# Kernel optimization log

Hardware: AMD Instinct MI355X
Metric: run time of the kernel (lower is better)

The kernel has to match this reference:

```python
import jax, jax.numpy as jnp
import numpy as np

N_NODES = 50000
N_EDGES = 800000
D_IN = 96
D_HID = 96


def _sage_conv(x, src, dst, Wl, b, Wr, n_nodes):
    # PyG SAGEConv (aggr='mean'): out = lin_l(mean_j x_j) + lin_r(x)
    msg = x[src]                                            # [E, d] gather
    agg = jax.ops.segment_sum(msg, dst, num_segments=n_nodes)
    cnt = jax.ops.segment_sum(jnp.ones((src.shape[0],), x.dtype), dst,
                              num_segments=n_nodes)
    agg = agg / jnp.maximum(cnt, 1.0)[:, None]              # mean (0 if no nbrs)
    return agg @ Wl.T + b + x @ Wr.T


def setup_inputs() -> dict:
    key = jax.random.key(0)
    ks = jax.random.split(key, 8)
    x = jax.random.normal(ks[0], (N_NODES, D_IN), dtype=jnp.float32)
    edge_index = jax.random.randint(ks[1], (2, N_EDGES), 0, N_NODES, dtype=jnp.int64)
    s1 = 1.0 / np.sqrt(D_IN)
    s2 = 1.0 / np.sqrt(D_HID)
    W1l = jax.random.uniform(ks[2], (D_HID, D_IN), jnp.float32, -s1, s1)
    b1 = jax.random.uniform(ks[3], (D_HID,), jnp.float32, -s1, s1)
    W1r = jax.random.uniform(ks[4], (D_HID, D_IN), jnp.float32, -s1, s1)
    W2l = jax.random.uniform(ks[5], (D_HID, D_HID), jnp.float32, -s2, s2)
    b2 = jax.random.uniform(ks[6], (D_HID,), jnp.float32, -s2, s2)
    W2r = jax.random.uniform(ks[7], (D_HID, D_HID), jnp.float32, -s2, s2)
    return {"x": x, "edge_index": edge_index, "W1l": W1l, "b1": b1,
            "W1r": W1r, "W2l": W2l, "b2": b2, "W2r": W2r}


def reference(x, edge_index, W1l, b1, W1r, W2l, b2, W2r):
    src, dst = edge_index[0], edge_index[1]
    n = x.shape[0]
    h = _sage_conv(x, src, dst, W1l, b1, W1r, n)   # conv1
    h = jax.nn.elu(h)
    h = _sage_conv(h, src, dst, W2l, b2, W2r, n)   # conv2
    return h
```

## Files before the change

kernel.cpp:

```cpp
#include <hip/hip_runtime.h>
#include <cmath>

#define N_NODES 50000
#define N_EDGES 800000
#define D 96

#define NB 1000
#define BN 50
#define SW 64
#define G 64
#define CHUNK ((N_EDGES + G - 1) / G)
#define PADB 16
#define CAP 4096

#define PACKW_BLOCKS 144
#define TOBF16_BLOCKS ((N_NODES * 96 / 4 + 255) / 256)

typedef __bf16 bf16x8 __attribute__((ext_vector_type(8)));
typedef float f32x4 __attribute__((ext_vector_type(4)));

__device__ inline float bflo(unsigned d) { return __uint_as_float(d << 16); }
__device__ inline float bfhi(unsigned d) { return __uint_as_float(d & 0xffff0000u); }
__device__ inline unsigned bfpack(float a, float b) {
  unsigned lo = (unsigned)__builtin_bit_cast(unsigned short, (__bf16)a);
  unsigned hi = (unsigned)__builtin_bit_cast(unsigned short, (__bf16)b);
  return lo | (hi << 16);
}

__global__ void __launch_bounds__(256)
k_prep(const int* __restrict__ dst, int* __restrict__ hist,
       const float* __restrict__ x, uint2* __restrict__ xbd,
       const float* __restrict__ W1l, const float* __restrict__ W1r,
       const float* __restrict__ W2l, const float* __restrict__ W2r,
       __bf16* __restrict__ Wp1, __bf16* __restrict__ Wp2) {
  __shared__ int h[NB];
  int tid = threadIdx.x, blk = blockIdx.x;
  if (blk < G) {
    int g = blk;
    for (int i = tid; i < NB; i += 256) h[i] = 0;
    __syncthreads();
    int e0 = g * CHUNK, e1 = min(e0 + CHUNK, N_EDGES);
    for (int e = e0 + tid; e < e1; e += 256) atomicAdd(&h[dst[e] / BN], 1);
    __syncthreads();
    for (int b = tid; b < NB; b += 256) hist[g * NB + b] = h[b];
  } else if (blk < G + PACKW_BLOCKS) {
    int w = blk - G;
    int set = w / 72;
    int i = (w % 72) * 256 + tid;
    const float* Wl = set ? W2l : W1l;
    const float* Wr = set ? W2r : W1r;
    __bf16* Wp = set ? Wp2 : Wp1;
    int f = i >> 9, r = i & 511;
    int l = r >> 3, j = r & 7;
    int t = f / 6, u = f % 6;
    int k = t * 32 + (l >> 4) * 8 + j;
    int d = u * 16 + (l & 15);
    float v = (k < 96) ? Wl[d * 96 + k] : Wr[d * 96 + (k - 96)];
    Wp[i] = (__bf16)v;
  } else {
    int i = (blk - G - PACKW_BLOCKS) * 256 + tid;
    if (i < N_NODES * 96 / 4) {
      float4 v = reinterpret_cast<const float4*>(x)[i];
      xbd[i] = make_uint2(bfpack(v.x, v.y), bfpack(v.z, v.w));
    }
  }
}

__global__ void k_chunkscan(const int* __restrict__ hist, int* __restrict__ chunkoff,
                            int* __restrict__ btot) {
  __shared__ int s[G];
  int b = blockIdx.x, g = threadIdx.x;
  int v = hist[g * NB + b];
  s[g] = v;
  __syncthreads();
#pragma unroll
  for (int d = 1; d < G; d <<= 1) {
    int t = (g >= d) ? s[g - d] : 0;
    __syncthreads();
    s[g] += t;
    __syncthreads();
  }
  chunkoff[b * G + g] = s[g] - v;
  if (g == G - 1) btot[b] = s[g];
}

__global__ void k_bscan(const int* __restrict__ btot, int* __restrict__ boffs) {
  __shared__ int s[1024];
  int i = threadIdx.x;
  int v = (i < NB) ? ((btot[i] + PADB - 1) & ~(PADB - 1)) : 0;
  s[i] = v;
  __syncthreads();
#pragma unroll
  for (int d = 1; d < 1024; d <<= 1) {
    int t = (i >= d) ? s[i - d] : 0;
    __syncthreads();
    s[i] += t;
    __syncthreads();
  }
  if (i < NB) boffs[i] = s[i] - v;
}

__global__ void k_scatter(const int* __restrict__ src, const int* __restrict__ dst,
                          const int* __restrict__ chunkoff, const int* __restrict__ boffs,
                          unsigned* __restrict__ pairs) {
  __shared__ int cur[NB];
  int tid = threadIdx.x, g = blockIdx.x;
  for (int b = tid; b < NB; b += 512) cur[b] = boffs[b] + chunkoff[b * G + g];
  __syncthreads();
  int e0 = g * CHUNK, e1 = min(e0 + CHUNK, N_EDGES);
  for (int e = e0 + tid; e < e1; e += 512) {
    int d = dst[e];
    int b = d / BN;
    int p = atomicAdd(&cur[b], 1);
    pairs[p] = (unsigned)src[e] | ((unsigned)(d - b * BN) << 16);
  }
}

__global__ void __launch_bounds__(512)
k_agg_fused(const unsigned* __restrict__ xind, const unsigned* __restrict__ pairs,
            const int* __restrict__ boffs, const int* __restrict__ btot,
            unsigned* __restrict__ aggd) {
  __shared__ int sorted[CAP];
  __shared__ int h[SW], seg[SW], cur[SW];
  int tid = threadIdx.x;
  int b = blockIdx.x;
  int c = tid >> 5, lane = tid & 31;
  bool act = lane < 24;
  int ebase = boffs[b];
  int ecnt = btot[b];

  float a0[4], a1[4], a2[4], a3[4];
  int ctot[4];
#pragma unroll
  for (int t = 0; t < 4; ++t) {
    a0[t] = a1[t] = a2[t] = a3[t] = 0.f;
    ctot[t] = 0;
  }

  for (int p0 = 0; p0 < ecnt; p0 += CAP) {
    int pcnt = min(CAP, ecnt - p0);
    if (tid < SW) h[tid] = 0;
    __syncthreads();
    for (int i = tid; i < pcnt; i += 512)
      atomicAdd(&h[pairs[ebase + p0 + i] >> 16], 1);
    __syncthreads();
    if (tid < SW) seg[tid] = h[tid];
    __syncthreads();
#pragma unroll
    for (int d = 1; d < SW; d <<= 1) {
      int t = 0;
      if (tid < SW && tid >= d) t = seg[tid - d];
      __syncthreads();
      if (tid < SW) seg[tid] += t;
      __syncthreads();
    }
    if (tid < SW) {
      int e = seg[tid] - h[tid];
      seg[tid] = e;
      cur[tid] = e;
    }
    __syncthreads();
    for (int i = tid; i < pcnt; i += 512) {
      unsigned pr = pairs[ebase + p0 + i];
      int q = atomicAdd(&cur[pr >> 16], 1);
      sorted[q] = (int)(pr & 0xffffu);
    }
    __syncthreads();
#pragma unroll
    for (int t = 0; t < 4; ++t) {
      int j = c + 16 * t;
      if (j < BN) {
        int st = seg[j], cn = h[j];
        if (act) {
          int i = 0;
          for (; i + 8 <= cn; i += 8) {
            uint2 u[8];
#pragma unroll
            for (int k = 0; k < 8; ++k) {
              int s = sorted[st + i + k];
              u[k] = reinterpret_cast<const uint2*>(xind + (size_t)s * 48)[lane];
            }
#pragma unroll
            for (int k = 0; k < 8; ++k) {
              a0[t] += bflo(u[k].x);
              a1[t] += bfhi(u[k].x);
              a2[t] += bflo(u[k].y);
              a3[t] += bfhi(u[k].y);
            }
          }
          for (; i + 2 <= cn; i += 2) {
            int s0 = sorted[st + i], s1 = sorted[st + i + 1];
            uint2 v0 = reinterpret_cast<const uint2*>(xind + (size_t)s0 * 48)[lane];
            uint2 v1 = reinterpret_cast<const uint2*>(xind + (size_t)s1 * 48)[lane];
            a0[t] += bflo(v0.x) + bflo(v1.x);
            a1[t] += bfhi(v0.x) + bfhi(v1.x);
            a2[t] += bflo(v0.y) + bflo(v1.y);
            a3[t] += bfhi(v0.y) + bfhi(v1.y);
          }
          for (; i < cn; ++i) {
            int s = sorted[st + i];
            uint2 v = reinterpret_cast<const uint2*>(xind + (size_t)s * 48)[lane];
            a0[t] += bflo(v.x);
            a1[t] += bfhi(v.x);
            a2[t] += bflo(v.y);
            a3[t] += bfhi(v.y);
          }
        }
        ctot[t] += cn;
      }
    }
    __syncthreads();
  }
#pragma unroll
  for (int t = 0; t < 4; ++t) {
    int j = c + 16 * t;
    if (j < BN && act) {
      int n = b * BN + j;
      float inv = 1.0f / fmaxf((float)ctot[t], 1.0f);
      uint2* o = reinterpret_cast<uint2*>(aggd + (size_t)n * 48);
      o[lane] = make_uint2(bfpack(a0[t] * inv, a1[t] * inv),
                           bfpack(a2[t] * inv, a3[t] * inv));
    }
  }
}

template <bool ELU, bool WRITE_BF16>
__global__ void __launch_bounds__(256, 2)
k_linear_mfma(const __bf16* __restrict__ A0, const __bf16* __restrict__ A1,
              const __bf16* __restrict__ Wp, const float* __restrict__ bias,
              float* __restrict__ outf, __bf16* __restrict__ outb) {
  int lane = threadIdx.x & 63;
  int wave = (blockIdx.x * blockDim.x + threadIdx.x) >> 6;
  int nwaves = (gridDim.x * blockDim.x) >> 6;

  bf16x8 B[36];
#pragma unroll
  for (int f = 0; f < 36; ++f)
    B[f] = *reinterpret_cast<const bf16x8*>(Wp + f * 512 + lane * 8);

  int col = lane & 15;
  int rowoff = (lane >> 4) * 4;
  int koff = (lane >> 4) * 8;
  float bv[6];
#pragma unroll
  for (int u = 0; u < 6; ++u) bv[u] = bias[u * 16 + col];

  const int NT = N_NODES / 16;
  for (int tile = wave; tile < NT; tile += nwaves) {
    int rowA = tile * 16 + (lane & 15);
    const __bf16* base0 = A0 + (size_t)rowA * 96 + koff;
    const __bf16* base1 = A1 + (size_t)rowA * 96 + koff;
    f32x4 acc[6];
#pragma unroll
    for (int u = 0; u < 6; ++u) acc[u] = (f32x4){0.f, 0.f, 0.f, 0.f};
#pragma unroll
    for (int t = 0; t < 3; ++t) {
      bf16x8 a = *reinterpret_cast<const bf16x8*>(base0 + t * 32);
#pragma unroll
      for (int u = 0; u < 6; ++u)
        acc[u] = __builtin_amdgcn_mfma_f32_16x16x32_bf16(a, B[t * 6 + u], acc[u], 0, 0, 0);
    }
#pragma unroll
    for (int t = 0; t < 3; ++t) {
      bf16x8 a = *reinterpret_cast<const bf16x8*>(base1 + t * 32);
#pragma unroll
      for (int u = 0; u < 6; ++u)
        acc[u] = __builtin_amdgcn_mfma_f32_16x16x32_bf16(a, B[(t + 3) * 6 + u], acc[u], 0, 0, 0);
    }
#pragma unroll
    for (int u = 0; u < 6; ++u) {
#pragma unroll
      for (int reg = 0; reg < 4; ++reg) {
        int r = tile * 16 + rowoff + reg;
        float v = acc[u][reg] + bv[u];
        if (ELU) v = (v > 0.f) ? v : expm1f(v);
        if (WRITE_BF16)
          outb[(size_t)r * 96 + u * 16 + col] = (__bf16)v;
        else
          outf[(size_t)r * 96 + u * 16 + col] = v;
      }
    }
  }
}


extern "C" void kernel_launch(void* const* d_in, const int* in_sizes, int n_in,
                              void* d_out, int out_size, void* d_ws, size_t ws_size,
                              hipStream_t stream) {
  const float* x = (const float*)d_in[0];
  const int* eidx = (const int*)d_in[1];
  const float* W1l = (const float*)d_in[2];
  const float* b1 = (const float*)d_in[3];
  const float* W1r = (const float*)d_in[4];
  const float* W2l = (const float*)d_in[5];
  const float* b2 = (const float*)d_in[6];
  const float* W2r = (const float*)d_in[7];
  float* out = (float*)d_out;

  const int* src = eidx;
  const int* dst = eidx + N_EDGES;

  char* w = (char*)d_ws;
  auto alloc = [&](size_t bytes) {
    char* p = w;
    w += (bytes + 255) & ~(size_t)255;
    return p;
  };
  int* hist = (int*)alloc((size_t)NB * G * 4);
  int* chunkoff = (int*)alloc((size_t)NB * G * 4);
  int* btot = (int*)alloc(NB * 4);
  int* boffs = (int*)alloc(NB * 4);
  unsigned* pairs = (unsigned*)alloc(((size_t)N_EDGES + (size_t)NB * PADB) * 4);
  __bf16* Wp1 = (__bf16*)alloc(36 * 512 * 2);
  __bf16* Wp2 = (__bf16*)alloc(36 * 512 * 2);
  __bf16* xb = (__bf16*)alloc((size_t)N_NODES * 96 * 2);
  __bf16* hb = (__bf16*)alloc((size_t)N_NODES * 96 * 2);
  __bf16* aggb = (__bf16*)alloc((size_t)N_NODES * 96 * 2);

  k_prep<<<G + PACKW_BLOCKS + TOBF16_BLOCKS, 256, 0, stream>>>(
      dst, hist, x, (uint2*)xb, W1l, W1r, W2l, W2r, Wp1, Wp2);
  k_chunkscan<<<NB, G, 0, stream>>>(hist, chunkoff, btot);
  k_bscan<<<1, 1024, 0, stream>>>(btot, boffs);
  k_scatter<<<G, 512, 0, stream>>>(src, dst, chunkoff, boffs, pairs);

  k_agg_fused<<<NB, 512, 0, stream>>>((const unsigned*)xb, pairs, boffs, btot, (unsigned*)aggb);
  k_linear_mfma<true, true><<<625, 256, 0, stream>>>(aggb, xb, Wp1, b1, nullptr, hb);
  k_agg_fused<<<NB, 512, 0, stream>>>((const unsigned*)hb, pairs, boffs, btot, (unsigned*)aggb);
  k_linear_mfma<false, false><<<625, 256, 0, stream>>>(aggb, hb, Wp2, b2, out, nullptr);
}
```

Measured before the change: 205.7 us.

## Build CSR in first aggregation and reuse it for the second layer

```diff
diff --git a/kernel.cpp b/kernel.cpp
--- a/kernel.cpp
+++ b/kernel.cpp
@@ -117,111 +117,117 @@
 }
 
 __global__ void __launch_bounds__(512)
-k_agg_fused(const unsigned* __restrict__ xind, const unsigned* __restrict__ pairs,
-            const int* __restrict__ boffs, const int* __restrict__ btot,
-            unsigned* __restrict__ aggd) {
-  __shared__ int sorted[CAP];
+k_agg_sort(const unsigned* __restrict__ xind, const unsigned* __restrict__ pairs,
+           const int* __restrict__ boffs, const int* __restrict__ btot,
+           unsigned* __restrict__ ssrc32, unsigned* __restrict__ nodeinfo,
+           unsigned* __restrict__ aggd) {
+  __shared__ unsigned short sorted[CAP + 2];
   __shared__ int h[SW], seg[SW], cur[SW];
+  int tid = threadIdx.x, b = blockIdx.x;
+  int ebase = boffs[b];
+  int ecnt = min(btot[b], CAP);
+  if (tid < SW) h[tid] = 0;
+  __syncthreads();
+  for (int i = tid; i < ecnt; i += 512)
+    atomicAdd(&h[pairs[ebase + i] >> 16], 1);
+  __syncthreads();
+  if (tid < SW) seg[tid] = h[tid];
+  __syncthreads();
+#pragma unroll
+  for (int d = 1; d < SW; d <<= 1) {
+    int t = 0;
+    if (tid < SW && tid >= d) t = seg[tid - d];
+    __syncthreads();
+    if (tid < SW) seg[tid] += t;
+    __syncthreads();
+  }
+  if (tid < SW) {
+    int e = seg[tid] - h[tid];
+    seg[tid] = e;
+    cur[tid] = e;
+  }
+  __syncthreads();
+  for (int i = tid; i < ecnt; i += 512) {
+    unsigned pr = pairs[ebase + i];
+    int q = atomicAdd(&cur[pr >> 16], 1);
+    sorted[q] = (unsigned short)(pr & 0xffffu);
+  }
+  if (tid == 0) sorted[ecnt] = 0;
+  __syncthreads();
+  for (int i = tid; i < (ecnt + 1) / 2; i += 512)
+    ssrc32[(ebase >> 1) + i] =
+        (unsigned)sorted[2 * i] | ((unsigned)sorted[2 * i + 1] << 16);
+  if (tid < BN)
+    nodeinfo[b * BN + tid] =
+        (unsigned)(ebase + seg[tid]) | ((unsigned)h[tid] << 20);
+  int c = tid >> 4, lane = tid & 15;
+  const uint3* xp = reinterpret_cast<const uint3*>(xind);
+  uint3* op = reinterpret_cast<uint3*>(aggd);
+  for (int j = c; j < BN; j += 32) {
+    int st = seg[j], cn = h[j];
+    float a0 = 0.f, a1 = 0.f, a2 = 0.f, a3 = 0.f, a4 = 0.f, a5 = 0.f;
+    int i = 0;
+    for (; i + 8 <= cn; i += 8) {
+      uint3 r[8];
+#pragma unroll
+      for (int k = 0; k < 8; ++k)
+        r[k] = xp[(size_t)sorted[st + i + k] * 16 + lane];
+#pragma unroll
+      for (int k = 0; k < 8; ++k) {
+        a0 += bflo(r[k].x); a1 += bfhi(r[k].x);
+        a2 += bflo(r[k].y); a3 += bfhi(r[k].y);
+        a4 += bflo(r[k].z); a5 += bfhi(r[k].z);
+      }
+    }
+    for (; i < cn; ++i) {
+      uint3 v = xp[(size_t)sorted[st + i] * 16 + lane];
+      a0 += bflo(v.x); a1 += bfhi(v.x);
+      a2 += bflo(v.y); a3 += bfhi(v.y);
+      a4 += bflo(v.z); a5 += bfhi(v.z);
+    }
+    float inv = 1.0f / fmaxf((float)cn, 1.0f);
+    op[(size_t)(b * BN + j) * 16 + lane] =
+        make_uint3(bfpack(a0 * inv, a1 * inv), bfpack(a2 * inv, a3 * inv),
+                   bfpack(a4 * inv, a5 * inv));
+  }
+}
+
+__global__ void __launch_bounds__(512)
+k_agg_csr(const unsigned* __restrict__ xind, const unsigned short* __restrict__ ssrc,
+          const unsigned* __restrict__ nodeinfo, unsigned* __restrict__ aggd) {
   int tid = threadIdx.x;
-  int b = blockIdx.x;
-  int c = tid >> 5, lane = tid & 31;
-  bool act = lane < 24;
-  int ebase = boffs[b];
-  int ecnt = btot[b];
-
-  float a0[4], a1[4], a2[4], a3[4];
-  int ctot[4];
-#pragma unroll
-  for (int t = 0; t < 4; ++t) {
-    a0[t] = a1[t] = a2[t] = a3[t] = 0.f;
-    ctot[t] = 0;
-  }
-
-  for (int p0 = 0; p0 < ecnt; p0 += CAP) {
-    int pcnt = min(CAP, ecnt - p0);
-    if (tid < SW) h[tid] = 0;
-    __syncthreads();
-    for (int i = tid; i < pcnt; i += 512)
-      atomicAdd(&h[pairs[ebase + p0 + i] >> 16], 1);
-    __syncthreads();
-    if (tid < SW) seg[tid] = h[tid];
-    __syncthreads();
-#pragma unroll
-    for (int d = 1; d < SW; d <<= 1) {
-      int t = 0;
-      if (tid < SW && tid >= d) t = seg[tid - d];
-      __syncthreads();
-      if (tid < SW) seg[tid] += t;
-      __syncthreads();
-    }
-    if (tid < SW) {
-      int e = seg[tid] - h[tid];
-      seg[tid] = e;
-      cur[tid] = e;
-    }
-    __syncthreads();
-    for (int i = tid; i < pcnt; i += 512) {
-      unsigned pr = pairs[ebase + p0 + i];
-      int q = atomicAdd(&cur[pr >> 16], 1);
-      sorted[q] = (int)(pr & 0xffffu);
-    }
-    __syncthreads();
-#pragma unroll
-    for (int t = 0; t < 4; ++t) {
-      int j = c + 16 * t;
-      if (j < BN) {
-        int st = seg[j], cn = h[j];
-        if (act) {
-          int i = 0;
-          for (; i + 8 <= cn; i += 8) {
-            uint2 u[8];
-#pragma unroll
-            for (int k = 0; k < 8; ++k) {
-              int s = sorted[st + i + k];
-              u[k] = reinterpret_cast<const uint2*>(xind + (size_t)s * 48)[lane];
-            }
-#pragma unroll
-            for (int k = 0; k < 8; ++k) {
-              a0[t] += bflo(u[k].x);
-              a1[t] += bfhi(u[k].x);
-              a2[t] += bflo(u[k].y);
-              a3[t] += bfhi(u[k].y);
-            }
-          }
-          for (; i + 2 <= cn; i += 2) {
-            int s0 = sorted[st + i], s1 = sorted[st + i + 1];
-            uint2 v0 = reinterpret_cast<const uint2*>(xind + (size_t)s0 * 48)[lane];
-            uint2 v1 = reinterpret_cast<const uint2*>(xind + (size_t)s1 * 48)[lane];
-            a0[t] += bflo(v0.x) + bflo(v1.x);
-            a1[t] += bfhi(v0.x) + bfhi(v1.x);
-            a2[t] += bflo(v0.y) + bflo(v1.y);
-            a3[t] += bfhi(v0.y) + bfhi(v1.y);
-          }
-          for (; i < cn; ++i) {
-            int s = sorted[st + i];
-            uint2 v = reinterpret_cast<const uint2*>(xind + (size_t)s * 48)[lane];
-            a0[t] += bflo(v.x);
-            a1[t] += bfhi(v.x);
-            a2[t] += bflo(v.y);
-            a3[t] += bfhi(v.y);
-          }
-        }
-        ctot[t] += cn;
-      }
-    }
-    __syncthreads();
-  }
-#pragma unroll
-  for (int t = 0; t < 4; ++t) {
-    int j = c + 16 * t;
-    if (j < BN && act) {
-      int n = b * BN + j;
-      float inv = 1.0f / fmaxf((float)ctot[t], 1.0f);
-      uint2* o = reinterpret_cast<uint2*>(aggd + (size_t)n * 48);
-      o[lane] = make_uint2(bfpack(a0[t] * inv, a1[t] * inv),
-                           bfpack(a2[t] * inv, a3[t] * inv));
-    }
-  }
+  int c = tid >> 4, lane = tid & 15;
+  int n = blockIdx.x * 32 + c;
+  if (n >= N_NODES) return;
+  unsigned info = nodeinfo[n];
+  int st = (int)(info & 0xFFFFFu);
+  int cn = (int)(info >> 20);
+  const uint3* xp = reinterpret_cast<const uint3*>(xind);
+  uint3* op = reinterpret_cast<uint3*>(aggd);
+  float a0 = 0.f, a1 = 0.f, a2 = 0.f, a3 = 0.f, a4 = 0.f, a5 = 0.f;
+  int i = 0;
+  for (; i + 8 <= cn; i += 8) {
+    uint3 r[8];
+#pragma unroll
+    for (int k = 0; k < 8; ++k)
+      r[k] = xp[(size_t)ssrc[st + i + k] * 16 + lane];
+#pragma unroll
+    for (int k = 0; k < 8; ++k) {
+      a0 += bflo(r[k].x); a1 += bfhi(r[k].x);
+      a2 += bflo(r[k].y); a3 += bfhi(r[k].y);
+      a4 += bflo(r[k].z); a5 += bfhi(r[k].z);
+    }
+  }
+  for (; i < cn; ++i) {
+    uint3 v = xp[(size_t)ssrc[st + i] * 16 + lane];
+    a0 += bflo(v.x); a1 += bfhi(v.x);
+    a2 += bflo(v.y); a3 += bfhi(v.y);
+    a4 += bflo(v.z); a5 += bfhi(v.z);
+  }
+  float inv = 1.0f / fmaxf((float)cn, 1.0f);
+  op[(size_t)n * 16 + lane] =
+      make_uint3(bfpack(a0 * inv, a1 * inv), bfpack(a2 * inv, a3 * inv),
+                 bfpack(a4 * inv, a5 * inv));
 }
 
 template <bool ELU, bool WRITE_BF16>
@@ -311,6 +317,8 @@
   int* btot = (int*)alloc(NB * 4);
   int* boffs = (int*)alloc(NB * 4);
   unsigned* pairs = (unsigned*)alloc(((size_t)N_EDGES + (size_t)NB * PADB) * 4);
+  unsigned* ssrc32 = (unsigned*)alloc(((size_t)N_EDGES + (size_t)NB * PADB + 2) * 2);
+  unsigned* nodeinfo = (unsigned*)alloc((size_t)N_NODES * 4);
   __bf16* Wp1 = (__bf16*)alloc(36 * 512 * 2);
   __bf16* Wp2 = (__bf16*)alloc(36 * 512 * 2);
   __bf16* xb = (__bf16*)alloc((size_t)N_NODES * 96 * 2);
@@ -323,8 +331,10 @@
   k_bscan<<<1, 1024, 0, stream>>>(btot, boffs);
   k_scatter<<<G, 512, 0, stream>>>(src, dst, chunkoff, boffs, pairs);
 
-  k_agg_fused<<<NB, 512, 0, stream>>>((const unsigned*)xb, pairs, boffs, btot, (unsigned*)aggb);
+  k_agg_sort<<<NB, 512, 0, stream>>>((const unsigned*)xb, pairs, boffs, btot,
+                                     ssrc32, nodeinfo, (unsigned*)aggb);
   k_linear_mfma<true, true><<<625, 256, 0, stream>>>(aggb, xb, Wp1, b1, nullptr, hb);
-  k_agg_fused<<<NB, 512, 0, stream>>>((const unsigned*)hb, pairs, boffs, btot, (unsigned*)aggb);
+  k_agg_csr<<<(N_NODES + 31) / 32, 512, 0, stream>>>(
+      (const unsigned*)hb, (const unsigned short*)ssrc32, nodeinfo, (unsigned*)aggb);
   k_linear_mfma<false, false><<<625, 256, 0, stream>>>(aggb, hb, Wp2, b2, out, nullptr);
 }
```

Result: faster. 192.7 us (-6.3%).
